# Performance work log

Measured on AMD Instinct MI355X. Metric: run time of the kernel, lower is better.

The kernel has to match this reference:

```python
import jax, jax.numpy as jnp
import numpy as np

B, N = 128, 512
REG = 0.1
EPS = 1e-20
TOL = 1e-3
SINKHORN_ITERS = 150
INIT_TEMP = 1.0
FINAL_TEMP = 0.1
NOISE_FACTOR = 0.015


def _gumbel(u, eps=1e-20):
    return -jnp.log(-jnp.log(u + eps) + eps)


def _concrete_sample(logits, u, tau):
    g = _gumbel(u)
    return jax.nn.softmax((logits + g) / tau, axis=-1)


def _stable_normalization(P):
    # Faithful to the torch code: prev_P is K = exp(-P0/reg), recomputed (constant)
    # every iteration; convergence break compares P against K.
    K = jnp.exp(-P / REG)

    def step(carry, _):
        P, done = carry
        row = jnp.sum(P, axis=-1, keepdims=True)
        Pn = P / jnp.where(row > EPS, row, 1.0)
        col = jnp.sum(Pn, axis=-2, keepdims=True)
        Pn = Pn / jnp.where(col > EPS, col, 1.0)
        Pn = jnp.clip(Pn, EPS, 1.0)
        diff = jnp.linalg.norm((Pn - K).ravel())
        # break happens AFTER the update, so the updated P is kept when converging
        P_out = jnp.where(done, P, Pn)
        done = done | (diff < TOL)
        return (P_out, done), None

    (P, _), _ = jax.lax.scan(step, (P, jnp.array(False)), None, length=SINKHORN_ITERS)
    return P


def setup_inputs() -> dict:
    key = jax.random.key(0)
    k1, k2, k3 = jax.random.split(key, 3)
    logits = jax.random.normal(k1, (B, N, N), dtype=jnp.float32)
    u1 = jax.random.uniform(k2, (B, N, N), dtype=jnp.float32)
    u2 = jax.random.uniform(k3, (B, N, N), dtype=jnp.float32)
    return {"logits": logits, "u1": u1, "u2": u2, "steps": 0}


def reference(logits, u1, u2, steps):
    temperature = max(INIT_TEMP * 0.9999 ** steps, FINAL_TEMP)
    g1 = _concrete_sample(logits, u1, temperature)
    g2 = _concrete_sample(logits, u2, 0.99)
    st = NOISE_FACTOR * g2
    # straight-through term: zero in the forward value, gradient flows through st
    noisy = logits + NOISE_FACTOR * g1 + (st - jax.lax.stop_gradient(st))
    P = jax.nn.softmax(noisy, axis=-1)
    return _stable_normalization(P)
```

## Files before the change

kernel.cpp:

```cpp
#include <hip/hip_runtime.h>
#include <math.h>

#define N_ 512
#define B_ 128
#define EPSV 1e-20f
#define ITERS 150
#define CONV_TOL 1e-5f

typedef __attribute__((ext_vector_type(8))) unsigned short ushort8;

static __device__ __forceinline__ float bf2f(unsigned short h) {
    union { unsigned int u; float f; } c; c.u = ((unsigned int)h) << 16; return c.f;
}
static __device__ __forceinline__ unsigned short f2bf(float f) {
    union { float f; unsigned int u; } c; c.f = f;
    unsigned int r = (c.u + 0x7FFFu + ((c.u >> 16) & 1u)) >> 16;
    return (unsigned short)r;
}
static __device__ __forceinline__ float frcp(float x) {
    return __builtin_amdgcn_rcpf(x);
}

template <bool BF16_OUT>
__global__ __launch_bounds__(256) void setup_kernel(
    const float* __restrict__ logits,
    const float* __restrict__ u1,
    const int* __restrict__ steps_p,
    float* __restrict__ P0f,
    unsigned short* __restrict__ P0h)
{
    const int wave = threadIdx.x >> 6;
    const int lane = threadIdx.x & 63;
    const int row  = (blockIdx.x << 2) + wave;
    const size_t base = (size_t)row * N_;

    const float stepsf = (float)(*steps_p);
    const float tau = fmaxf(__expf(stepsf * -1.0000500033e-4f), 0.1f);
    const float inv_tau = frcp(tau);

    const float4* Lp = (const float4*)(logits + base);
    const float4* Up = (const float4*)(u1 + base);
    const float4 l0 = Lp[2 * lane], l1 = Lp[2 * lane + 1];
    const float4 q0 = Up[2 * lane], q1 = Up[2 * lane + 1];
    float L[8] = {l0.x, l0.y, l0.z, l0.w, l1.x, l1.y, l1.z, l1.w};
    float U[8] = {q0.x, q0.y, q0.z, q0.w, q1.x, q1.y, q1.z, q1.w};

    float x[8];
    #pragma unroll
    for (int k = 0; k < 8; ++k) {
        float g = -__logf(-__logf(U[k] + 1e-20f) + 1e-20f);
        x[k] = (L[k] + g) * inv_tau;
    }

    float m = x[0];
    #pragma unroll
    for (int k = 1; k < 8; ++k) m = fmaxf(m, x[k]);
    #pragma unroll
    for (int off = 32; off; off >>= 1) m = fmaxf(m, __shfl_xor(m, off));

    float e[8], s = 0.0f;
    #pragma unroll
    for (int k = 0; k < 8; ++k) { e[k] = __expf(x[k] - m); s += e[k]; }
    #pragma unroll
    for (int off = 32; off; off >>= 1) s += __shfl_xor(s, off);
    const float rZ1 = frcp(s);

    float y[8];
    #pragma unroll
    for (int k = 0; k < 8; ++k) y[k] = L[k] + 0.015f * (e[k] * rZ1);

    float m2 = y[0];
    #pragma unroll
    for (int k = 1; k < 8; ++k) m2 = fmaxf(m2, y[k]);
    #pragma unroll
    for (int off = 32; off; off >>= 1) m2 = fmaxf(m2, __shfl_xor(m2, off));

    float f[8], z = 0.0f;
    #pragma unroll
    for (int k = 0; k < 8; ++k) { f[k] = __expf(y[k] - m2); z += f[k]; }
    #pragma unroll
    for (int off = 32; off; off >>= 1) z += __shfl_xor(z, off);
    const float rZ2 = frcp(z);

    if (BF16_OUT) {
        ushort8 o;
        #pragma unroll
        for (int k = 0; k < 8; ++k) o[k] = f2bf(f[k] * rZ2);
        *(ushort8*)(P0h + base + (lane << 3)) = o;
    } else {
        const int c0 = lane << 3;
        float4* dst = (float4*)(P0f + base + c0);
        dst[0] = make_float4(f[0]*rZ2, f[1]*rZ2, f[2]*rZ2, f[3]*rZ2);
        dst[1] = make_float4(f[4]*rZ2, f[5]*rZ2, f[6]*rZ2, f[7]*rZ2);
    }
}

__global__ __launch_bounds__(1024) void sinkhorn_bf16(
    const unsigned short* __restrict__ Pb, float* __restrict__ Out)
{
    const int b = blockIdx.x;
    const unsigned short* __restrict__ M = Pb + (size_t)b * N_ * N_;
    float* __restrict__ O = Out + (size_t)b * N_ * N_;

    const int tid = threadIdx.x;
    const int lane = tid & 63;
    const int wave = tid >> 6;
    const int c0 = lane << 3;
    const int rbase = wave << 5;

    __shared__ float u_s[N_];
    __shared__ float v_s[N_];
    __shared__ float cpart[16][N_];
    __shared__ float wmax[8];

    if (tid < N_) { u_s[tid] = 1.0f; v_s[tid] = 1.0f; }
    __syncthreads();

    for (int it = 0; it < ITERS; ++it) {
        float vr[8];
        #pragma unroll
        for (int k = 0; k < 8; ++k) vr[k] = v_s[c0 + k];
        float colacc[8] = {0.f,0.f,0.f,0.f,0.f,0.f,0.f,0.f};

        #pragma unroll 4
        for (int rr = 0; rr < 32; ++rr) {
            const int r = rbase + rr;
            ushort8 h = *(const ushort8*)(M + ((size_t)r << 9) + c0);
            float x[8];
            #pragma unroll
            for (int k = 0; k < 8; ++k) x[k] = bf2f(h[k]);
            float d = x[0]*vr[0] + x[1]*vr[1] + x[2]*vr[2] + x[3]*vr[3]
                    + x[4]*vr[4] + x[5]*vr[5] + x[6]*vr[6] + x[7]*vr[7];
            #pragma unroll
            for (int off = 32; off; off >>= 1) d += __shfl_xor(d, off);
            const float uo = u_s[r];
            const float un = (uo * d > EPSV) ? frcp(d) : uo;
            if (lane == 0) u_s[r] = un;
            #pragma unroll
            for (int k = 0; k < 8; ++k) colacc[k] += x[k] * un;
        }
        #pragma unroll
        for (int k = 0; k < 8; ++k) cpart[wave][c0 + k] = colacc[k];
        __syncthreads();

        float mrel = 0.0f;
        if (tid < N_) {
            float c = 0.0f;
            #pragma unroll
            for (int w = 0; w < 16; ++w) c += cpart[w][tid];
            const float vo = v_s[tid];
            const float vn = (vo * c > EPSV) ? frcp(c) : vo;
            v_s[tid] = vn;
            mrel = fabsf(vn - vo) * frcp(vo);
        }
        #pragma unroll
        for (int off = 32; off; off >>= 1) mrel = fmaxf(mrel, __shfl_xor(mrel, off));
        if (lane == 0 && wave < 8) wmax[wave] = mrel;
        __syncthreads();

        float mx = wmax[0];
        #pragma unroll
        for (int w = 1; w < 8; ++w) mx = fmaxf(mx, wmax[w]);
        if (mx < CONV_TOL) break;
    }

    float vrf[8];
    #pragma unroll
    for (int k = 0; k < 8; ++k) vrf[k] = v_s[c0 + k];
    for (int rr = 0; rr < 32; ++rr) {
        const int r = rbase + rr;
        ushort8 h = *(const ushort8*)(M + ((size_t)r << 9) + c0);
        const float ur = u_s[r];
        float o[8];
        #pragma unroll
        for (int k = 0; k < 8; ++k)
            o[k] = fminf(fmaxf(bf2f(h[k]) * ur * vrf[k], EPSV), 1.0f);
        float4* dst = (float4*)(O + ((size_t)r << 9) + c0);
        dst[0] = make_float4(o[0], o[1], o[2], o[3]);
        dst[1] = make_float4(o[4], o[5], o[6], o[7]);
    }
}

__global__ __launch_bounds__(1024) void sinkhorn_f32(float* __restrict__ P)
{
    const int b = blockIdx.x;
    float* __restrict__ M = P + (size_t)b * N_ * N_;
    float4* __restrict__ M4 = (float4*)M;

    const int tid = threadIdx.x;
    const int lane = tid & 63;
    const int wave = tid >> 6;
    const int jb = tid & 127;
    const int rq = tid >> 7;

    __shared__ float4 u4s[N_ / 4];
    __shared__ float4 v4s[N_ / 4];
    __shared__ float4 cpartf[1024];
    float* u = (float*)u4s;
    float* v = (float*)v4s;

    if (tid < N_) { u[tid] = 1.0f; v[tid] = 1.0f; }
    __syncthreads();

    for (int it = 0; it < ITERS; ++it) {
        for (int r = wave; r < N_; r += 16) {
            const float4* row4 = M4 + (size_t)r * (N_ / 4);
            float4 a = row4[lane];
            float4 bq = row4[lane + 64];
            float4 va = v4s[lane];
            float4 vb = v4s[lane + 64];
            float acc = a.x*va.x + a.y*va.y + a.z*va.z + a.w*va.w
                      + bq.x*vb.x + bq.y*vb.y + bq.z*vb.z + bq.w*vb.w;
            #pragma unroll
            for (int off = 32; off; off >>= 1) acc += __shfl_xor(acc, off);
            if (lane == 0) {
                float uo = u[r];
                u[r] = (uo * acc > EPSV) ? (1.0f / acc) : uo;
            }
        }
        __syncthreads();

        float4 acc4 = make_float4(0.f, 0.f, 0.f, 0.f);
        for (int r = rq; r < N_; r += 8) {
            float4 mrow = M4[(size_t)r * (N_ / 4) + jb];
            float ur = u[r];
            acc4.x += mrow.x * ur; acc4.y += mrow.y * ur;
            acc4.z += mrow.z * ur; acc4.w += mrow.w * ur;
        }
        cpartf[tid] = acc4;
        __syncthreads();
        if (tid < 128) {
            float4 cs = cpartf[tid];
            #pragma unroll
            for (int k = 1; k < 8; ++k) {
                float4 p = cpartf[tid + (k << 7)];
                cs.x += p.x; cs.y += p.y; cs.z += p.z; cs.w += p.w;
            }
            float vo0 = v[4*tid+0], vo1 = v[4*tid+1], vo2 = v[4*tid+2], vo3 = v[4*tid+3];
            v[4*tid+0] = (vo0 * cs.x > EPSV) ? (1.0f / cs.x) : vo0;
            v[4*tid+1] = (vo1 * cs.y > EPSV) ? (1.0f / cs.y) : vo1;
            v[4*tid+2] = (vo2 * cs.z > EPSV) ? (1.0f / cs.z) : vo2;
            v[4*tid+3] = (vo3 * cs.w > EPSV) ? (1.0f / cs.w) : vo3;
        }
        __syncthreads();
    }

    for (int r = rq; r < N_; r += 8) {
        size_t idx = (size_t)r * (N_ / 4) + jb;
        float4 mrow = M4[idx];
        float ur = u[r];
        float4 vv = v4s[jb];
        mrow.x = fminf(fmaxf(mrow.x * ur * vv.x, EPSV), 1.0f);
        mrow.y = fminf(fmaxf(mrow.y * ur * vv.y, EPSV), 1.0f);
        mrow.z = fminf(fmaxf(mrow.z * ur * vv.z, EPSV), 1.0f);
        mrow.w = fminf(fmaxf(mrow.w * ur * vv.w, EPSV), 1.0f);
        M4[idx] = mrow;
    }
}

extern "C" void kernel_launch(void* const* d_in, const int* in_sizes, int n_in,
                              void* d_out, int out_size, void* d_ws, size_t ws_size,
                              hipStream_t stream) {
    const float* logits = (const float*)d_in[0];
    const float* u1     = (const float*)d_in[1];
    const int* steps    = (const int*)d_in[3];
    float* out = (float*)d_out;

    const size_t need = (size_t)B_ * N_ * N_ * sizeof(unsigned short);

    if (ws_size >= need) {
        unsigned short* P0h = (unsigned short*)d_ws;
        setup_kernel<true><<<B_ * N_ / 4, 256, 0, stream>>>(logits, u1, steps, nullptr, P0h);
        sinkhorn_bf16<<<B_, 1024, 0, stream>>>(P0h, out);
    } else {
        setup_kernel<false><<<B_ * N_ / 4, 256, 0, stream>>>(logits, u1, steps, out, nullptr);
        sinkhorn_f32<<<B_, 1024, 0, stream>>>(out);
    }
}
```

Before: 183.5 us.

## Fuse setup into register-resident Sinkhorn split across paired blocks with flag exchange

Merges the softmax setup and the Sinkhorn loop into one kernel. Each matrix is split across two workgroups that each hold 256 rows in registers as bf16, so the bf16 workspace round trip and the per-iteration global reloads go away. Column sums are exchanged between the paired blocks every iteration through global memory, using release/acquire flags and a spin-wait. This adds inter-block synchronisation latency per iteration and assumes all 256 blocks are co-resident, otherwise the spin-wait deadlocks. It also adds a memset launch.

```diff
diff --git a/kernel.cpp b/kernel.cpp
--- a/kernel.cpp
+++ b/kernel.cpp
@@ -21,13 +21,185 @@
     return __builtin_amdgcn_rcpf(x);
 }
 
-template <bool BF16_OUT>
-__global__ __launch_bounds__(256) void setup_kernel(
+__global__ __launch_bounds__(1024) void fused_sinkhorn(
     const float* __restrict__ logits,
     const float* __restrict__ u1,
     const int* __restrict__ steps_p,
-    float* __restrict__ P0f,
-    unsigned short* __restrict__ P0h)
+    float* __restrict__ Out,
+    float* __restrict__ exch,
+    int* __restrict__ flags)
+{
+    const int b    = blockIdx.x;
+    const int mat  = b & 127;
+    const int half = b >> 7;
+    const int tid  = threadIdx.x;
+    const int lane = tid & 63;
+    const int wave = tid >> 6;
+    const int c0   = lane << 3;
+
+    __shared__ float u_s[256];
+    __shared__ float v_s[N_];
+    __shared__ float cpart[16][N_];
+    __shared__ float cloc[N_];
+    __shared__ float wmax[8];
+
+    const float stepsf  = (float)(*steps_p);
+    const float inv_tau = frcp(fmaxf(__expf(stepsf * -1.0000500033e-4f), 0.1f));
+
+    ushort8 Mreg[16];
+    #pragma unroll
+    for (int rr = 0; rr < 16; ++rr) {
+        const int g = (half << 8) + (wave << 4) + rr;
+        const size_t base = ((size_t)mat << 18) + ((size_t)g << 9);
+        const float4 l0 = *(const float4*)(logits + base + c0);
+        const float4 l1 = *(const float4*)(logits + base + c0 + 4);
+        const float4 q0 = *(const float4*)(u1 + base + c0);
+        const float4 q1 = *(const float4*)(u1 + base + c0 + 4);
+        float L[8] = {l0.x,l0.y,l0.z,l0.w,l1.x,l1.y,l1.z,l1.w};
+        float U[8] = {q0.x,q0.y,q0.z,q0.w,q1.x,q1.y,q1.z,q1.w};
+
+        float x[8];
+        #pragma unroll
+        for (int k = 0; k < 8; ++k) {
+            const float gg = -__logf(-__logf(U[k] + 1e-20f) + 1e-20f);
+            x[k] = (L[k] + gg) * inv_tau;
+        }
+        float m = x[0];
+        #pragma unroll
+        for (int k = 1; k < 8; ++k) m = fmaxf(m, x[k]);
+        #pragma unroll
+        for (int off = 32; off; off >>= 1) m = fmaxf(m, __shfl_xor(m, off));
+
+        float e[8], s = 0.0f;
+        #pragma unroll
+        for (int k = 0; k < 8; ++k) { e[k] = __expf(x[k] - m); s += e[k]; }
+        #pragma unroll
+        for (int off = 32; off; off >>= 1) s += __shfl_xor(s, off);
+        const float rZ1 = frcp(s);
+
+        float y[8];
+        #pragma unroll
+        for (int k = 0; k < 8; ++k) y[k] = L[k] + 0.015f * (e[k] * rZ1);
+
+        float m2 = y[0];
+        #pragma unroll
+        for (int k = 1; k < 8; ++k) m2 = fmaxf(m2, y[k]);
+        #pragma unroll
+        for (int off = 32; off; off >>= 1) m2 = fmaxf(m2, __shfl_xor(m2, off));
+
+        float f[8], z = 0.0f;
+        #pragma unroll
+        for (int k = 0; k < 8; ++k) { f[k] = __expf(y[k] - m2); z += f[k]; }
+        #pragma unroll
+        for (int off = 32; off; off >>= 1) z += __shfl_xor(z, off);
+        const float rZ2 = frcp(z);
+
+        ushort8 o;
+        #pragma unroll
+        for (int k = 0; k < 8; ++k) o[k] = f2bf(f[k] * rZ2);
+        Mreg[rr] = o;
+    }
+
+    if (tid < 256) u_s[tid] = 1.0f;
+    if (tid < N_)  v_s[tid] = 1.0f;
+    __syncthreads();
+
+    float* const my_ex = exch + (((size_t)mat * 2 + half) << 10);
+    float* const pa_ex = exch + (((size_t)mat * 2 + (1 - half)) << 10);
+    int* const my_fl = flags + (mat * 2 + half);
+    int* const pa_fl = flags + (mat * 2 + (1 - half));
+
+    for (int it = 0; it < ITERS; ++it) {
+        float vr[8];
+        #pragma unroll
+        for (int k = 0; k < 8; ++k) vr[k] = v_s[c0 + k];
+        float colacc[8] = {0.f,0.f,0.f,0.f,0.f,0.f,0.f,0.f};
+
+        #pragma unroll
+        for (int rr = 0; rr < 16; ++rr) {
+            const int r = (wave << 4) + rr;
+            const ushort8 h = Mreg[rr];
+            float x[8];
+            #pragma unroll
+            for (int k = 0; k < 8; ++k) x[k] = bf2f(h[k]);
+            float d = x[0]*vr[0] + x[1]*vr[1] + x[2]*vr[2] + x[3]*vr[3]
+                    + x[4]*vr[4] + x[5]*vr[5] + x[6]*vr[6] + x[7]*vr[7];
+            #pragma unroll
+            for (int off = 32; off; off >>= 1) d += __shfl_xor(d, off);
+            const float uo = u_s[r];
+            const float un = (uo * d > EPSV) ? frcp(d) : uo;
+            if (lane == 0) u_s[r] = un;
+            #pragma unroll
+            for (int k = 0; k < 8; ++k) colacc[k] += x[k] * un;
+        }
+        #pragma unroll
+        for (int k = 0; k < 8; ++k) cpart[wave][c0 + k] = colacc[k];
+        __syncthreads();
+
+        if (tid < N_) {
+            float c = 0.0f;
+            #pragma unroll
+            for (int w = 0; w < 16; ++w) c += cpart[w][tid];
+            cloc[tid] = c;
+            __hip_atomic_store(&my_ex[((it & 1) << 9) + tid], c,
+                               __ATOMIC_RELAXED, __HIP_MEMORY_SCOPE_AGENT);
+            __threadfence();
+        }
+        __syncthreads();
+
+        if (tid == 0) {
+            __hip_atomic_store(my_fl, it + 1, __ATOMIC_RELEASE, __HIP_MEMORY_SCOPE_AGENT);
+            while (__hip_atomic_load(pa_fl, __ATOMIC_ACQUIRE, __HIP_MEMORY_SCOPE_AGENT) < it + 1) {
+                __builtin_amdgcn_s_sleep(1);
+            }
+        }
+        __syncthreads();
+
+        float mrel = 0.0f;
+        if (tid < N_) {
+            const float cp = __hip_atomic_load(&pa_ex[((it & 1) << 9) + tid],
+                                               __ATOMIC_RELAXED, __HIP_MEMORY_SCOPE_AGENT);
+            const float c = cloc[tid] + cp;
+            const float vo = v_s[tid];
+            const float vn = (vo * c > EPSV) ? frcp(c) : vo;
+            v_s[tid] = vn;
+            mrel = fabsf(vn - vo) * frcp(vo);
+        }
+        #pragma unroll
+        for (int off = 32; off; off >>= 1) mrel = fmaxf(mrel, __shfl_xor(mrel, off));
+        if (lane == 0 && wave < 8) wmax[wave] = mrel;
+        __syncthreads();
+
+        float mx = wmax[0];
+        #pragma unroll
+        for (int w = 1; w < 8; ++w) mx = fmaxf(mx, wmax[w]);
+        if (mx < CONV_TOL) break;
+    }
+
+    float vrf[8];
+    #pragma unroll
+    for (int k = 0; k < 8; ++k) vrf[k] = v_s[c0 + k];
+    #pragma unroll
+    for (int rr = 0; rr < 16; ++rr) {
+        const int r = (wave << 4) + rr;
+        const int g = (half << 8) + r;
+        const ushort8 h = Mreg[rr];
+        const float ur = u_s[r];
+        float o[8];
+        #pragma unroll
+        for (int k = 0; k < 8; ++k)
+            o[k] = fminf(fmaxf(bf2f(h[k]) * ur * vrf[k], EPSV), 1.0f);
+        float4* dst = (float4*)(Out + ((size_t)mat << 18) + ((size_t)g << 9) + c0);
+        dst[0] = make_float4(o[0], o[1], o[2], o[3]);
+        dst[1] = make_float4(o[4], o[5], o[6], o[7]);
+    }
+}
+
+__global__ __launch_bounds__(256) void setup_f32(
+    const float* __restrict__ logits,
+    const float* __restrict__ u1,
+    const int* __restrict__ steps_p,
+    float* __restrict__ P0f)
 {
     const int wave = threadIdx.x >> 6;
     const int lane = threadIdx.x & 63;
@@ -35,15 +207,14 @@
     const size_t base = (size_t)row * N_;
 
     const float stepsf = (float)(*steps_p);
-    const float tau = fmaxf(__expf(stepsf * -1.0000500033e-4f), 0.1f);
-    const float inv_tau = frcp(tau);
+    const float inv_tau = frcp(fmaxf(__expf(stepsf * -1.0000500033e-4f), 0.1f));
 
     const float4* Lp = (const float4*)(logits + base);
     const float4* Up = (const float4*)(u1 + base);
-    const float4 l0 = Lp[2 * lane], l1 = Lp[2 * lane + 1];
-    const float4 q0 = Up[2 * lane], q1 = Up[2 * lane + 1];
-    float L[8] = {l0.x, l0.y, l0.z, l0.w, l1.x, l1.y, l1.z, l1.w};
-    float U[8] = {q0.x, q0.y, q0.z, q0.w, q1.x, q1.y, q1.z, q1.w};
+    const float4 l0 = Lp[2*lane], l1 = Lp[2*lane+1];
+    const float4 q0 = Up[2*lane], q1 = Up[2*lane+1];
+    float L[8] = {l0.x,l0.y,l0.z,l0.w,l1.x,l1.y,l1.z,l1.w};
+    float U[8] = {q0.x,q0.y,q0.z,q0.w,q1.x,q1.y,q1.z,q1.w};
 
     float x[8];
     #pragma unroll
@@ -51,30 +222,25 @@
         float g = -__logf(-__logf(U[k] + 1e-20f) + 1e-20f);
         x[k] = (L[k] + g) * inv_tau;
     }
-
     float m = x[0];
     #pragma unroll
     for (int k = 1; k < 8; ++k) m = fmaxf(m, x[k]);
     #pragma unroll
     for (int off = 32; off; off >>= 1) m = fmaxf(m, __shfl_xor(m, off));
-
     float e[8], s = 0.0f;
     #pragma unroll
     for (int k = 0; k < 8; ++k) { e[k] = __expf(x[k] - m); s += e[k]; }
     #pragma unroll
     for (int off = 32; off; off >>= 1) s += __shfl_xor(s, off);
     const float rZ1 = frcp(s);
-
     float y[8];
     #pragma unroll
     for (int k = 0; k < 8; ++k) y[k] = L[k] + 0.015f * (e[k] * rZ1);
-
     float m2 = y[0];
     #pragma unroll
     for (int k = 1; k < 8; ++k) m2 = fmaxf(m2, y[k]);
     #pragma unroll
     for (int off = 32; off; off >>= 1) m2 = fmaxf(m2, __shfl_xor(m2, off));
-
     float f[8], z = 0.0f;
     #pragma unroll
     for (int k = 0; k < 8; ++k) { f[k] = __expf(y[k] - m2); z += f[k]; }
@@ -82,103 +248,10 @@
     for (int off = 32; off; off >>= 1) z += __shfl_xor(z, off);
     const float rZ2 = frcp(z);
 
-    if (BF16_OUT) {
-        ushort8 o;
-        #pragma unroll
-        for (int k = 0; k < 8; ++k) o[k] = f2bf(f[k] * rZ2);
-        *(ushort8*)(P0h + base + (lane << 3)) = o;
-    } else {
-        const int c0 = lane << 3;
-        float4* dst = (float4*)(P0f + base + c0);
-        dst[0] = make_float4(f[0]*rZ2, f[1]*rZ2, f[2]*rZ2, f[3]*rZ2);
-        dst[1] = make_float4(f[4]*rZ2, f[5]*rZ2, f[6]*rZ2, f[7]*rZ2);
-    }
-}
-
-__global__ __launch_bounds__(1024) void sinkhorn_bf16(
-    const unsigned short* __restrict__ Pb, float* __restrict__ Out)
-{
-    const int b = blockIdx.x;
-    const unsigned short* __restrict__ M = Pb + (size_t)b * N_ * N_;
-    float* __restrict__ O = Out + (size_t)b * N_ * N_;
-
-    const int tid = threadIdx.x;
-    const int lane = tid & 63;
-    const int wave = tid >> 6;
     const int c0 = lane << 3;
-    const int rbase = wave << 5;
-
-    __shared__ float u_s[N_];
-    __shared__ float v_s[N_];
-    __shared__ float cpart[16][N_];
-    __shared__ float wmax[8];
-
-    if (tid < N_) { u_s[tid] = 1.0f; v_s[tid] = 1.0f; }
-    __syncthreads();
-
-    for (int it = 0; it < ITERS; ++it) {
-        float vr[8];
-        #pragma unroll
-        for (int k = 0; k < 8; ++k) vr[k] = v_s[c0 + k];
-        float colacc[8] = {0.f,0.f,0.f,0.f,0.f,0.f,0.f,0.f};
-
-        #pragma unroll 4
-        for (int rr = 0; rr < 32; ++rr) {
-            const int r = rbase + rr;
-            ushort8 h = *(const ushort8*)(M + ((size_t)r << 9) + c0);
-            float x[8];
-            #pragma unroll
-            for (int k = 0; k < 8; ++k) x[k] = bf2f(h[k]);
-            float d = x[0]*vr[0] + x[1]*vr[1] + x[2]*vr[2] + x[3]*vr[3]
-                    + x[4]*vr[4] + x[5]*vr[5] + x[6]*vr[6] + x[7]*vr[7];
-            #pragma unroll
-            for (int off = 32; off; off >>= 1) d += __shfl_xor(d, off);
-            const float uo = u_s[r];
-            const float un = (uo * d > EPSV) ? frcp(d) : uo;
-            if (lane == 0) u_s[r] = un;
-            #pragma unroll
-            for (int k = 0; k < 8; ++k) colacc[k] += x[k] * un;
-        }
-        #pragma unroll
-        for (int k = 0; k < 8; ++k) cpart[wave][c0 + k] = colacc[k];
-        __syncthreads();
-
-        float mrel = 0.0f;
-        if (tid < N_) {
-            float c = 0.0f;
-            #pragma unroll
-            for (int w = 0; w < 16; ++w) c += cpart[w][tid];
-            const float vo = v_s[tid];
-            const float vn = (vo * c > EPSV) ? frcp(c) : vo;
-            v_s[tid] = vn;
-            mrel = fabsf(vn - vo) * frcp(vo);
-        }
-        #pragma unroll
-        for (int off = 32; off; off >>= 1) mrel = fmaxf(mrel, __shfl_xor(mrel, off));
-        if (lane == 0 && wave < 8) wmax[wave] = mrel;
-        __syncthreads();
-
-        float mx = wmax[0];
-        #pragma unroll
-        for (int w = 1; w < 8; ++w) mx = fmaxf(mx, wmax[w]);
-        if (mx < CONV_TOL) break;
-    }
-
-    float vrf[8];
-    #pragma unroll
-    for (int k = 0; k < 8; ++k) vrf[k] = v_s[c0 + k];
-    for (int rr = 0; rr < 32; ++rr) {
-        const int r = rbase + rr;
-        ushort8 h = *(const ushort8*)(M + ((size_t)r << 9) + c0);
-        const float ur = u_s[r];
-        float o[8];
-        #pragma unroll
-        for (int k = 0; k < 8; ++k)
-            o[k] = fminf(fmaxf(bf2f(h[k]) * ur * vrf[k], EPSV), 1.0f);
-        float4* dst = (float4*)(O + ((size_t)r << 9) + c0);
-        dst[0] = make_float4(o[0], o[1], o[2], o[3]);
-        dst[1] = make_float4(o[4], o[5], o[6], o[7]);
-    }
+    float4* dst = (float4*)(P0f + base + c0);
+    dst[0] = make_float4(f[0]*rZ2, f[1]*rZ2, f[2]*rZ2, f[3]*rZ2);
+    dst[1] = make_float4(f[4]*rZ2, f[5]*rZ2, f[6]*rZ2, f[7]*rZ2);
 }
 
 __global__ __launch_bounds__(1024) void sinkhorn_f32(float* __restrict__ P)
@@ -266,14 +339,15 @@
     const int* steps    = (const int*)d_in[3];
     float* out = (float*)d_out;
 
-    const size_t need = (size_t)B_ * N_ * N_ * sizeof(unsigned short);
+    const size_t need = 4096 + (size_t)B_ * 2 * 2 * N_ * sizeof(float);
 
     if (ws_size >= need) {
-        unsigned short* P0h = (unsigned short*)d_ws;
-        setup_kernel<true><<<B_ * N_ / 4, 256, 0, stream>>>(logits, u1, steps, nullptr, P0h);
-        sinkhorn_bf16<<<B_, 1024, 0, stream>>>(P0h, out);
+        int*   flags = (int*)d_ws;
+        float* exch  = (float*)((char*)d_ws + 4096);
+        hipMemsetAsync(d_ws, 0, 4096, stream);
+        fused_sinkhorn<<<2 * B_, 1024, 0, stream>>>(logits, u1, steps, out, exch, flags);
     } else {
-        setup_kernel<false><<<B_ * N_ / 4, 256, 0, stream>>>(logits, u1, steps, out, nullptr);
+        setup_f32<<<B_ * N_ / 4, 256, 0, stream>>>(logits, u1, steps, out);
         sinkhorn_f32<<<B_, 1024, 0, stream>>>(out);
     }
 }
```

After: 545.5 us. +197.2%, slower.

## Add FP8 copy of the matrix for Sinkhorn iterations and loosen convergence tolerance

Applied to the files above, without the earlier changes.

The setup kernel now also writes a scaled FP8 (e4m3-style) copy of the softmax matrix alongside the bf16 copy. The Sinkhorn scaling iterations stream the FP8 copy, halving the bytes read per iteration, and the final output pass still uses the bf16 copy. The early-exit tolerance is raised from 1e-5 to 1e-4, so iteration can stop sooner. Both changes trade accuracy of the scaling vectors for bandwidth and iteration count, and the setup kernel writes an extra buffer.

```diff
diff --git a/kernel.cpp b/kernel.cpp
--- a/kernel.cpp
+++ b/kernel.cpp
@@ -5,7 +5,8 @@
 #define B_ 128
 #define EPSV 1e-20f
 #define ITERS 150
-#define CONV_TOL 1e-5f
+#define CONV_TOL 1e-4f
+#define INV512 0.001953125f
 
 typedef __attribute__((ext_vector_type(8))) unsigned short ushort8;
 
@@ -21,13 +22,45 @@
     return __builtin_amdgcn_rcpf(x);
 }
 
-template <bool BF16_OUT>
+static __device__ __forceinline__ unsigned char f2fp8(float w) {
+    if (w >= 0.015625f) {
+        unsigned int b = __float_as_uint(w);
+        unsigned int r = b + 0x7FFFFu + ((b >> 20) & 1u);
+        return (unsigned char)((r >> 20) - 960u);
+    }
+    return (unsigned char)__float2int_rn(w * 512.0f);
+}
+
+static __device__ __forceinline__ void fp8x8_dec(unsigned int wlo, unsigned int whi, float* f) {
+#if defined(__has_builtin) && __has_builtin(__builtin_amdgcn_cvt_f32_fp8)
+    f[0] = __builtin_amdgcn_cvt_f32_fp8(wlo, 0);
+    f[1] = __builtin_amdgcn_cvt_f32_fp8(wlo, 1);
+    f[2] = __builtin_amdgcn_cvt_f32_fp8(wlo, 2);
+    f[3] = __builtin_amdgcn_cvt_f32_fp8(wlo, 3);
+    f[4] = __builtin_amdgcn_cvt_f32_fp8(whi, 0);
+    f[5] = __builtin_amdgcn_cvt_f32_fp8(whi, 1);
+    f[6] = __builtin_amdgcn_cvt_f32_fp8(whi, 2);
+    f[7] = __builtin_amdgcn_cvt_f32_fp8(whi, 3);
+#else
+    #pragma unroll
+    for (int k = 0; k < 4; ++k) {
+        unsigned int s0 = wlo >> (8 * k), s1 = whi >> (8 * k);
+        float a, b;
+        asm volatile("v_cvt_f32_fp8 %0, %1" : "=v"(a) : "v"(s0));
+        asm volatile("v_cvt_f32_fp8 %0, %1" : "=v"(b) : "v"(s1));
+        f[k] = a; f[4 + k] = b;
+    }
+#endif
+}
+
+template <int MODE>
 __global__ __launch_bounds__(256) void setup_kernel(
     const float* __restrict__ logits,
     const float* __restrict__ u1,
     const int* __restrict__ steps_p,
     float* __restrict__ P0f,
-    unsigned short* __restrict__ P0h)
+    unsigned short* __restrict__ P0h,
+    unsigned char* __restrict__ P8)
 {
     const int wave = threadIdx.x >> 6;
     const int lane = threadIdx.x & 63;
@@ -35,15 +68,14 @@
     const size_t base = (size_t)row * N_;
 
     const float stepsf = (float)(*steps_p);
-    const float tau = fmaxf(__expf(stepsf * -1.0000500033e-4f), 0.1f);
-    const float inv_tau = frcp(tau);
+    const float inv_tau = frcp(fmaxf(__expf(stepsf * -1.0000500033e-4f), 0.1f));
 
     const float4* Lp = (const float4*)(logits + base);
     const float4* Up = (const float4*)(u1 + base);
-    const float4 l0 = Lp[2 * lane], l1 = Lp[2 * lane + 1];
-    const float4 q0 = Up[2 * lane], q1 = Up[2 * lane + 1];
-    float L[8] = {l0.x, l0.y, l0.z, l0.w, l1.x, l1.y, l1.z, l1.w};
-    float U[8] = {q0.x, q0.y, q0.z, q0.w, q1.x, q1.y, q1.z, q1.w};
+    const float4 l0 = Lp[2*lane], l1 = Lp[2*lane+1];
+    const float4 q0 = Up[2*lane], q1 = Up[2*lane+1];
+    float L[8] = {l0.x,l0.y,l0.z,l0.w,l1.x,l1.y,l1.z,l1.w};
+    float U[8] = {q0.x,q0.y,q0.z,q0.w,q1.x,q1.y,q1.z,q1.w};
 
     float x[8];
     #pragma unroll
@@ -51,30 +83,25 @@
         float g = -__logf(-__logf(U[k] + 1e-20f) + 1e-20f);
         x[k] = (L[k] + g) * inv_tau;
     }
-
     float m = x[0];
     #pragma unroll
     for (int k = 1; k < 8; ++k) m = fmaxf(m, x[k]);
     #pragma unroll
     for (int off = 32; off; off >>= 1) m = fmaxf(m, __shfl_xor(m, off));
-
     float e[8], s = 0.0f;
     #pragma unroll
     for (int k = 0; k < 8; ++k) { e[k] = __expf(x[k] - m); s += e[k]; }
     #pragma unroll
     for (int off = 32; off; off >>= 1) s += __shfl_xor(s, off);
     const float rZ1 = frcp(s);
-
     float y[8];
     #pragma unroll
     for (int k = 0; k < 8; ++k) y[k] = L[k] + 0.015f * (e[k] * rZ1);
-
     float m2 = y[0];
     #pragma unroll
     for (int k = 1; k < 8; ++k) m2 = fmaxf(m2, y[k]);
     #pragma unroll
     for (int off = 32; off; off >>= 1) m2 = fmaxf(m2, __shfl_xor(m2, off));
-
     float f[8], z = 0.0f;
     #pragma unroll
     for (int k = 0; k < 8; ++k) { f[k] = __expf(y[k] - m2); z += f[k]; }
@@ -82,25 +109,38 @@
     for (int off = 32; off; off >>= 1) z += __shfl_xor(z, off);
     const float rZ2 = frcp(z);
 
-    if (BF16_OUT) {
-        ushort8 o;
-        #pragma unroll
-        for (int k = 0; k < 8; ++k) o[k] = f2bf(f[k] * rZ2);
-        *(ushort8*)(P0h + base + (lane << 3)) = o;
-    } else {
-        const int c0 = lane << 3;
+    const int c0 = lane << 3;
+    if (MODE == 0) {
         float4* dst = (float4*)(P0f + base + c0);
         dst[0] = make_float4(f[0]*rZ2, f[1]*rZ2, f[2]*rZ2, f[3]*rZ2);
         dst[1] = make_float4(f[4]*rZ2, f[5]*rZ2, f[6]*rZ2, f[7]*rZ2);
-    }
-}
-
-__global__ __launch_bounds__(1024) void sinkhorn_bf16(
-    const unsigned short* __restrict__ Pb, float* __restrict__ Out)
+    } else {
+        float p[8];
+        ushort8 o;
+        #pragma unroll
+        for (int k = 0; k < 8; ++k) { p[k] = f[k] * rZ2; o[k] = f2bf(p[k]); }
+        *(ushort8*)(P0h + base + c0) = o;
+        if (MODE == 2) {
+            unsigned int lo = 0, hi = 0;
+            #pragma unroll
+            for (int k = 0; k < 4; ++k) {
+                lo |= ((unsigned int)f2fp8(p[k]     * 512.0f)) << (8 * k);
+                hi |= ((unsigned int)f2fp8(p[4 + k] * 512.0f)) << (8 * k);
+            }
+            *(uint2*)(P8 + base + c0) = make_uint2(lo, hi);
+        }
+    }
+}
+
+__global__ __launch_bounds__(1024) void sinkhorn_fp8(
+    const unsigned char* __restrict__ P8,
+    const unsigned short* __restrict__ Pb,
+    float* __restrict__ Out)
 {
     const int b = blockIdx.x;
-    const unsigned short* __restrict__ M = Pb + (size_t)b * N_ * N_;
-    float* __restrict__ O = Out + (size_t)b * N_ * N_;
+    const unsigned char* __restrict__ M8 = P8 + ((size_t)b << 18);
+    const unsigned short* __restrict__ Mh = Pb + ((size_t)b << 18);
+    float* __restrict__ O = Out + ((size_t)b << 18);
 
     const int tid = threadIdx.x;
     const int lane = tid & 63;
@@ -120,7 +160,94 @@
         float vr[8];
         #pragma unroll
         for (int k = 0; k < 8; ++k) vr[k] = v_s[c0 + k];
-        float colacc[8] = {0.f,0.f,0.f,0.f,0.f,0.f,0.f,0.f};
+        float ca[8] = {0.f,0.f,0.f,0.f,0.f,0.f,0.f,0.f};
+
+        #pragma unroll 4
+        for (int rr = 0; rr < 32; ++rr) {
+            const int r = rbase + rr;
+            const uint2 W = *(const uint2*)(M8 + ((size_t)r << 9) + c0);
+            float x[8];
+            fp8x8_dec(W.x, W.y, x);
+            float d = x[0]*vr[0] + x[1]*vr[1] + x[2]*vr[2] + x[3]*vr[3]
+                    + x[4]*vr[4] + x[5]*vr[5] + x[6]*vr[6] + x[7]*vr[7];
+            #pragma unroll
+            for (int off = 32; off; off >>= 1) d += __shfl_xor(d, off);
+            const float dt = d * INV512;
+            const float uo = u_s[r];
+            const float un = (uo * dt > EPSV) ? frcp(dt) : uo;
+            if (lane == 0) u_s[r] = un;
+            #pragma unroll
+            for (int k = 0; k < 8; ++k) ca[k] += x[k] * un;
+        }
+        #pragma unroll
+        for (int k = 0; k < 8; ++k) cpart[wave][c0 + k] = ca[k];
+        __syncthreads();
+
+        float mrel = 0.0f;
+        if (tid < N_) {
+            float c = 0.0f;
+            #pragma unroll
+            for (int w = 0; w < 16; ++w) c += cpart[w][tid];
+            const float ct = c * INV512;
+            const float vo = v_s[tid];
+            const float vn = (vo * ct > EPSV) ? frcp(ct) : vo;
+            v_s[tid] = vn;
+            mrel = fabsf(vn - vo) * frcp(vo);
+        }
+        #pragma unroll
+        for (int off = 32; off; off >>= 1) mrel = fmaxf(mrel, __shfl_xor(mrel, off));
+        if (lane == 0 && wave < 8) wmax[wave] = mrel;
+        __syncthreads();
+
+        float mx = wmax[0];
+        #pragma unroll
+        for (int w = 1; w < 8; ++w) mx = fmaxf(mx, wmax[w]);
+        if (mx < CONV_TOL) break;
+    }
+
+    float vrf[8];
+    #pragma unroll
+    for (int k = 0; k < 8; ++k) vrf[k] = v_s[c0 + k];
+    for (int rr = 0; rr < 32; ++rr) {
+        const int r = rbase + rr;
+        ushort8 h = *(const ushort8*)(Mh + ((size_t)r << 9) + c0);
+        const float ur = u_s[r];
+        float o[8];
+        #pragma unroll
+        for (int k = 0; k < 8; ++k)
+            o[k] = fminf(fmaxf(bf2f(h[k]) * ur * vrf[k], EPSV), 1.0f);
+        float4* dst = (float4*)(O + ((size_t)r << 9) + c0);
+        dst[0] = make_float4(o[0], o[1], o[2], o[3]);
+        dst[1] = make_float4(o[4], o[5], o[6], o[7]);
+    }
+}
+
+__global__ __launch_bounds__(1024) void sinkhorn_bf16(
+    const unsigned short* __restrict__ Pb, float* __restrict__ Out)
+{
+    const int b = blockIdx.x;
+    const unsigned short* __restrict__ M = Pb + ((size_t)b << 18);
+    float* __restrict__ O = Out + ((size_t)b << 18);
+
+    const int tid = threadIdx.x;
+    const int lane = tid & 63;
+    const int wave = tid >> 6;
+    const int c0 = lane << 3;
+    const int rbase = wave << 5;
+
+    __shared__ float u_s[N_];
+    __shared__ float v_s[N_];
+    __shared__ float cpart[16][N_];
+    __shared__ float wmax[8];
+
+    if (tid < N_) { u_s[tid] = 1.0f; v_s[tid] = 1.0f; }
+    __syncthreads();
+
+    for (int it = 0; it < ITERS; ++it) {
+        float vr[8];
+        #pragma unroll
+        for (int k = 0; k < 8; ++k) vr[k] = v_s[c0 + k];
+        float ca[8] = {0.f,0.f,0.f,0.f,0.f,0.f,0.f,0.f};
 
         #pragma unroll 4
         for (int rr = 0; rr < 32; ++rr) {
@@ -137,10 +264,10 @@
             const float un = (uo * d > EPSV) ? frcp(d) : uo;
             if (lane == 0) u_s[r] = un;
             #pragma unroll
-            for (int k = 0; k < 8; ++k) colacc[k] += x[k] * un;
-        }
-        #pragma unroll
-        for (int k = 0; k < 8; ++k) cpart[wave][c0 + k] = colacc[k];
+            for (int k = 0; k < 8; ++k) ca[k] += x[k] * un;
+        }
+        #pragma unroll
+        for (int k = 0; k < 8; ++k) cpart[wave][c0 + k] = ca[k];
         __syncthreads();
 
         float mrel = 0.0f;
@@ -266,14 +393,21 @@
     const int* steps    = (const int*)d_in[3];
     float* out = (float*)d_out;
 
-    const size_t need = (size_t)B_ * N_ * N_ * sizeof(unsigned short);
-
-    if (ws_size >= need) {
+    const size_t nelem = (size_t)B_ * N_ * N_;
+    const size_t need_fp8  = nelem * 2 + nelem;
+    const size_t need_bf16 = nelem * 2;
+
+    if (ws_size >= need_fp8) {
         unsigned short* P0h = (unsigned short*)d_ws;
-        setup_kernel<true><<<B_ * N_ / 4, 256, 0, stream>>>(logits, u1, steps, nullptr, P0h);
+        unsigned char*  P8  = (unsigned char*)d_ws + nelem * 2;
+        setup_kernel<2><<<B_ * N_ / 4, 256, 0, stream>>>(logits, u1, steps, nullptr, P0h, P8);
+        sinkhorn_fp8<<<B_, 1024, 0, stream>>>(P8, P0h, out);
+    } else if (ws_size >= need_bf16) {
+        unsigned short* P0h = (unsigned short*)d_ws;
+        setup_kernel<1><<<B_ * N_ / 4, 256, 0, stream>>>(logits, u1, steps, nullptr, P0h, nullptr);
         sinkhorn_bf16<<<B_, 1024, 0, stream>>>(P0h, out);
     } else {
-        setup_kernel<false><<<B_ * N_ / 4, 256, 0, stream>>>(logits, u1, steps, out, nullptr);
+        setup_kernel<0><<<B_ * N_ / 4, 256, 0, stream>>>(logits, u1, steps, out, nullptr, nullptr);
         sinkhorn_f32<<<B_, 1024, 0, stream>>>(out);
     }
 }
```

After: 188.3 us. 1.03x slower.
